# Kernel tuning notes

Measured on AMD Instinct MI355X. Metric: run time of the kernel, lower is better.

## Reference

```python
import jax, jax.numpy as jnp
import numpy as np

BLOCK_SIZE = 256
N_EMBD = 384
NUM_BLOCKS = 3
N_HEADS = 6
VOCAB_SIZE = 65
HEAD = N_EMBD // N_HEADS
EPS = 1e-5


def setup_inputs() -> dict:
    key = jax.random.key(0)
    ks = jax.random.split(key, 20)
    B, T = 64, 256
    s = 0.02
    L = NUM_BLOCKS
    inp = {
        "idx": jax.random.randint(ks[0], (B, T), 0, VOCAB_SIZE),
        "tok_emb": jax.random.normal(ks[1], (VOCAB_SIZE, N_EMBD), jnp.float32) * s,
        "pos_emb": jax.random.normal(ks[2], (BLOCK_SIZE, N_EMBD), jnp.float32) * s,
        "Wq": jax.random.normal(ks[3], (L, N_EMBD, N_EMBD), jnp.float32) * s,
        "Wk": jax.random.normal(ks[4], (L, N_EMBD, N_EMBD), jnp.float32) * s,
        "Wv": jax.random.normal(ks[5], (L, N_EMBD, N_EMBD), jnp.float32) * s,
        "Wo": jax.random.normal(ks[6], (L, N_EMBD, N_EMBD), jnp.float32) * s,
        "bo": jnp.zeros((L, N_EMBD), jnp.float32),
        "ln1_g": jnp.ones((L, N_EMBD), jnp.float32),
        "ln1_b": jnp.zeros((L, N_EMBD), jnp.float32),
        "ln2_g": jnp.ones((L, N_EMBD), jnp.float32),
        "ln2_b": jnp.zeros((L, N_EMBD), jnp.float32),
        "W1": jax.random.normal(ks[7], (L, N_EMBD, 4 * N_EMBD), jnp.float32) * s,
        "b1": jnp.zeros((L, 4 * N_EMBD), jnp.float32),
        "W2": jax.random.normal(ks[8], (L, 4 * N_EMBD, N_EMBD), jnp.float32) * s,
        "b2": jnp.zeros((L, N_EMBD), jnp.float32),
        "lnf_g": jnp.ones((N_EMBD,), jnp.float32),
        "lnf_b": jnp.zeros((N_EMBD,), jnp.float32),
        "Wlm": jax.random.normal(ks[9], (N_EMBD, VOCAB_SIZE), jnp.float32) * s,
        "blm": jnp.zeros((VOCAB_SIZE,), jnp.float32),
    }
    return inp


def _ln(x, g, b):
    m = jnp.mean(x, axis=-1, keepdims=True)
    v = jnp.mean((x - m) ** 2, axis=-1, keepdims=True)
    return (x - m) * jax.lax.rsqrt(v + EPS) * g + b


def reference(idx, tok_emb, pos_emb, Wq, Wk, Wv, Wo, bo, ln1_g, ln1_b,
              ln2_g, ln2_b, W1, b1, W2, b2, lnf_g, lnf_b, Wlm, blm):
    B, T = idx.shape
    x = tok_emb[idx] + pos_emb[:T]  # [B,T,C]
    scale = N_EMBD ** (-0.5)  # NOTE: original scales by full C=N_EMBD, not head_size
    causal = jnp.tril(jnp.ones((T, T), bool))
    neg_inf = jnp.finfo(x.dtype).min
    for l in range(NUM_BLOCKS):
        h = _ln(x, ln1_g[l], ln1_b[l])
        q = (h @ Wq[l]).reshape(B, T, N_HEADS, HEAD)
        k = (h @ Wk[l]).reshape(B, T, N_HEADS, HEAD)
        v = (h @ Wv[l]).reshape(B, T, N_HEADS, HEAD)
        wei = jnp.einsum("bthd,bshd->bhts", q, k) * scale
        wei = jnp.where(causal, wei, neg_inf)
        wei = jax.nn.softmax(wei, axis=-1)  # dropout is identity in eval
        att = jnp.einsum("bhts,bshd->bthd", wei, v).reshape(B, T, N_EMBD)
        x = x + att @ Wo[l] + bo[l]
        h2 = _ln(x, ln2_g[l], ln2_b[l])
        x = x + jax.nn.relu(h2 @ W1[l] + b1[l]) @ W2[l] + b2[l]
    x = _ln(x, lnf_g, lnf_b)
    logits = x @ Wlm + blm  # [B,T,V]
    return logits
```

## Files before the change

kernel.cpp:

```cpp
#include <hip/hip_runtime.h>

#define Bb 64
#define Tt 256
#define Cc 384
#define Ll 3
#define Hh 6
#define HD 64
#define Vv 65
#define FF 1536
#define NT (Bb*Tt)
#define CQ 1152
#define LDP 72

typedef unsigned short u16;
typedef unsigned int   u32;
typedef __attribute__((ext_vector_type(8))) short bf16x8;
typedef __attribute__((ext_vector_type(4))) float f32x4;

__device__ __forceinline__ float bf2f(u16 u) {
    u32 v = ((u32)u) << 16; float f; __builtin_memcpy(&f, &v, 4); return f;
}
__device__ __forceinline__ u16 f2bf(float f) {
    u32 u; __builtin_memcpy(&u, &f, 4);
    u = (u + 0x7fffu + ((u >> 16) & 1u)) >> 16;
    return (u16)u;
}
__device__ __forceinline__ void gload16(const void* g, void* l) {
    __builtin_amdgcn_global_load_lds(
        (const __attribute__((address_space(1))) u32*)g,
        (__attribute__((address_space(3))) u32*)l, 16, 0, 0);
}

__global__ __launch_bounds__(256) void k_embed_ln(const int* __restrict__ idx,
    const float* __restrict__ tok, const float* __restrict__ pos,
    const float* __restrict__ g, const float* __restrict__ b,
    float* __restrict__ x, u16* __restrict__ h)
{
    int bt   = (int)((blockIdx.x * 256 + threadIdx.x) >> 6);
    int lane = threadIdx.x & 63;
    int t = bt % Tt;
    const float* tr = tok + (long)idx[bt] * Cc;
    const float* pr = pos + (long)t * Cc;
    float v[6]; float s = 0.f;
    #pragma unroll
    for (int j = 0; j < 6; ++j) {
        int c = lane + 64 * j;
        v[j] = tr[c] + pr[c];
        s += v[j];
    }
    float* xr = x + (long)bt * Cc;
    #pragma unroll
    for (int j = 0; j < 6; ++j) xr[lane + 64 * j] = v[j];
    #pragma unroll
    for (int m = 32; m; m >>= 1) s += __shfl_xor(s, m, 64);
    float mean = s * (1.f / 384.f);
    float q = 0.f;
    #pragma unroll
    for (int j = 0; j < 6; ++j) { float d = v[j] - mean; q += d * d; }
    #pragma unroll
    for (int m = 32; m; m >>= 1) q += __shfl_xor(q, m, 64);
    float rstd = rsqrtf(q * (1.f / 384.f) + 1e-5f);
    u16* hr = h + (long)bt * Cc;
    #pragma unroll
    for (int j = 0; j < 6; ++j) {
        int c = lane + 64 * j;
        hr[c] = f2bf((v[j] - mean) * rstd * g[c] + b[c]);
    }
}

__global__ __launch_bounds__(256) void k_ln(const float* __restrict__ x,
    const float* __restrict__ g, const float* __restrict__ b, u16* __restrict__ h)
{
    int row  = (int)((blockIdx.x * 256 + threadIdx.x) >> 6);
    int lane = threadIdx.x & 63;
    const float* xr = x + (long)row * Cc;
    float v[6]; float s = 0.f;
    #pragma unroll
    for (int j = 0; j < 6; ++j) { v[j] = xr[lane + 64 * j]; s += v[j]; }
    #pragma unroll
    for (int m = 32; m; m >>= 1) s += __shfl_xor(s, m, 64);
    float mean = s * (1.f / 384.f);
    float q = 0.f;
    #pragma unroll
    for (int j = 0; j < 6; ++j) { float d = v[j] - mean; q += d * d; }
    #pragma unroll
    for (int m = 32; m; m >>= 1) q += __shfl_xor(q, m, 64);
    float rstd = rsqrtf(q * (1.f / 384.f) + 1e-5f);
    u16* hr = h + (long)row * Cc;
    #pragma unroll
    for (int j = 0; j < 6; ++j) {
        int c = lane + 64 * j;
        hr[c] = f2bf((v[j] - mean) * rstd * g[c] + b[c]);
    }
}

__global__ __launch_bounds__(256) void k_cvtT_all(
    const float* __restrict__ Wq, const float* __restrict__ Wk,
    const float* __restrict__ Wv, const float* __restrict__ Wo,
    const float* __restrict__ W1, const float* __restrict__ W2,
    u16* __restrict__ Wqkvt, u16* __restrict__ Wot,
    u16* __restrict__ W1t, u16* __restrict__ W2t)
{
    int t = blockIdx.x;
    const float* src; u16* dst; int K, N, tt;
    if (t < 1728) {
        int m = t / 144; tt = t % 144; K = Cc; N = Cc;
        if (m < 9) {
            int l = m / 3, q = m % 3;
            src = (q == 0 ? Wq : q == 1 ? Wk : Wv) + (size_t)l * Cc * Cc;
            dst = Wqkvt + (size_t)l * CQ * Cc + (size_t)q * Cc * Cc;
        } else {
            int l = m - 9;
            src = Wo + (size_t)l * Cc * Cc;
            dst = Wot + (size_t)l * Cc * Cc;
        }
    } else if (t < 3456) {
        int u = t - 1728; int l = u / 576; tt = u % 576; K = Cc; N = FF;
        src = W1 + (size_t)l * Cc * FF; dst = W1t + (size_t)l * FF * Cc;
    } else {
        int u = t - 3456; int l = u / 576; tt = u % 576; K = FF; N = Cc;
        src = W2 + (size_t)l * FF * Cc; dst = W2t + (size_t)l * Cc * FF;
    }
    int nk = K / 32;
    int kt = (tt % nk) * 32, nt = (tt / nk) * 32;
    __shared__ u16 tile[32][33];
    int tx = threadIdx.x & 31, ty = threadIdx.x >> 5;
    #pragma unroll
    for (int r = 0; r < 4; ++r)
        tile[ty + 8 * r][tx] = f2bf(src[(long)(kt + ty + 8 * r) * N + nt + tx]);
    __syncthreads();
    #pragma unroll
    for (int r = 0; r < 4; ++r)
        dst[(long)(nt + ty + 8 * r) * K + kt + tx] = tile[tx][ty + 8 * r];
}

__global__ void k_cvtT_lm(const float* __restrict__ W, u16* __restrict__ Wt)
{
    int i = blockIdx.x * 256 + threadIdx.x;
    if (i >= 128 * Cc) return;
    int k = i % Cc, n = i / Cc;
    Wt[i] = (n < Vv) ? f2bf(W[(long)k * Vv + n]) : (u16)0;
}

template<int EPI>
__global__ __launch_bounds__(256) void k_gemm128(
    const u16* __restrict__ A, const u16* __restrict__ Bt,
    const float* __restrict__ bias, void* __restrict__ Cout, int M, int N, int K)
{
    __shared__ __align__(16) u16 As[128 * 64];
    __shared__ __align__(16) u16 Bs[128 * 64];
    const int bm = blockIdx.x * 128;
    const int bn = blockIdx.y * 128;
    const int tid = threadIdx.x;
    const int lane = tid & 63, w = tid >> 6;
    const int wr = w >> 1, wc = w & 1;
    const int l15 = lane & 15, g = lane >> 4;
    const int lr = lane >> 3;
    const int lc = ((lane & 7) ^ lr) * 8;

    f32x4 acc[4][4] = {};
    const u16* Ag = A  + (long)(bm + w * 32 + lr) * K + lc;
    const u16* Bg = Bt + (long)(bn + w * 32 + lr) * K + lc;
    u16* Ad = As + (w * 4) * 512;
    u16* Bd = Bs + (w * 4) * 512;

    for (int k0 = 0; k0 < K; k0 += 64) {
        #pragma unroll
        for (int s = 0; s < 4; ++s) {
            gload16(Ag + (long)s * 8 * K + k0, Ad + s * 512);
            gload16(Bg + (long)s * 8 * K + k0, Bd + s * 512);
        }
        __syncthreads();
        #pragma unroll
        for (int hh = 0; hh < 2; ++hh) {
            const int cs = hh * 4 + g;
            bf16x8 af[4], bfr[4];
            #pragma unroll
            for (int mi = 0; mi < 4; ++mi) {
                int row = wr * 64 + mi * 16 + l15;
                af[mi] = *(const bf16x8*)((const char*)As + row * 128 + ((cs ^ (row & 7)) << 4));
            }
            #pragma unroll
            for (int ni = 0; ni < 4; ++ni) {
                int row = wc * 64 + ni * 16 + l15;
                bfr[ni] = *(const bf16x8*)((const char*)Bs + row * 128 + ((cs ^ (row & 7)) << 4));
            }
            #pragma unroll
            for (int mi = 0; mi < 4; ++mi)
            #pragma unroll
            for (int ni = 0; ni < 4; ++ni)
                acc[mi][ni] = __builtin_amdgcn_mfma_f32_16x16x32_bf16(af[mi], bfr[ni], acc[mi][ni], 0, 0, 0);
        }
        __syncthreads();
    }
    #pragma unroll
    for (int mi = 0; mi < 4; ++mi)
    #pragma unroll
    for (int ni = 0; ni < 4; ++ni)
    #pragma unroll
    for (int i = 0; i < 4; ++i) {
        int row = bm + wr * 64 + mi * 16 + g * 4 + i;
        int col = bn + wc * 64 + ni * 16 + l15;
        float v = acc[mi][ni][i];
        if constexpr (EPI == 1) v = fmaxf(v + bias[col], 0.f);
        ((u16*)Cout)[(long)row * N + col] = f2bf(v);
    }
}

template<int EPI>
__global__ __launch_bounds__(256) void k_gemm_n64(
    const u16* __restrict__ A, const u16* __restrict__ Bt,
    const float* __restrict__ bias, const float* __restrict__ R,
    void* __restrict__ Cout, int M, int N, int K, int Nout)
{
    __shared__ __align__(16) u16 As[128 * 64];
    __shared__ __align__(16) u16 Bs[64 * 64];
    const int bm = blockIdx.x * 128;
    const int bn = blockIdx.y * 64;
    const int tid = threadIdx.x;
    const int lane = tid & 63, w = tid >> 6;
    const int l15 = lane & 15, g = lane >> 4;
    const int lr = lane >> 3;
    const int lc = ((lane & 7) ^ lr) * 8;

    f32x4 acc[2][4] = {};
    const u16* Ag = A  + (long)(bm + w * 32 + lr) * K + lc;
    const u16* Bg = Bt + (long)(bn + w * 16 + lr) * K + lc;
    u16* Ad = As + (w * 4) * 512;
    u16* Bd = Bs + (w * 2) * 512;

    for (int k0 = 0; k0 < K; k0 += 64) {
        #pragma unroll
        for (int s = 0; s < 4; ++s)
            gload16(Ag + (long)s * 8 * K + k0, Ad + s * 512);
        #pragma unroll
        for (int t = 0; t < 2; ++t)
            gload16(Bg + (long)t * 8 * K + k0, Bd + t * 512);
        __syncthreads();
        #pragma unroll
        for (int hh = 0; hh < 2; ++hh) {
            const int cs = hh * 4 + g;
            bf16x8 af[2], bfr[4];
            #pragma unroll
            for (int mi = 0; mi < 2; ++mi) {
                int row = w * 32 + mi * 16 + l15;
                af[mi] = *(const bf16x8*)((const char*)As + row * 128 + ((cs ^ (row & 7)) << 4));
            }
            #pragma unroll
            for (int ni = 0; ni < 4; ++ni) {
                int row = ni * 16 + l15;
                bfr[ni] = *(const bf16x8*)((const char*)Bs + row * 128 + ((cs ^ (row & 7)) << 4));
            }
            #pragma unroll
            for (int mi = 0; mi < 2; ++mi)
            #pragma unroll
            for (int ni = 0; ni < 4; ++ni)
                acc[mi][ni] = __builtin_amdgcn_mfma_f32_16x16x32_bf16(af[mi], bfr[ni], acc[mi][ni], 0, 0, 0);
        }
        __syncthreads();
    }
    #pragma unroll
    for (int mi = 0; mi < 2; ++mi)
    #pragma unroll
    for (int ni = 0; ni < 4; ++ni)
    #pragma unroll
    for (int i = 0; i < 4; ++i) {
        int row = bm + w * 32 + mi * 16 + g * 4 + i;
        int col = bn + ni * 16 + l15;
        float v = acc[mi][ni][i];
        if constexpr (EPI == 2) {
            long o = (long)row * N + col;
            ((float*)Cout)[o] = v + bias[col] + R[o];
        } else {
            if (col < Nout)
                ((float*)Cout)[(long)row * Nout + col] = v + bias[col];
        }
    }
}

__global__ __launch_bounds__(256) void k_attn_mfma(const u16* __restrict__ qkv,
                                                   u16* __restrict__ att)
{
    __shared__ __align__(16) u16 ks[64][LDP];
    __shared__ __align__(16) u16 vt[64][LDP];
    __shared__ __align__(16) u16 pt[4][16][LDP];
    const int qt = blockIdx.x, hh = blockIdx.y, b = blockIdx.z;
    const int tid = threadIdx.x, lane = tid & 63, w = tid >> 6;
    const int l15 = lane & 15, g = lane >> 4;
    const int q0 = qt * 64;
    const long tokbase = (long)b * Tt;
    const float scale = 0.051031036307982884f;

    bf16x8 qa0, qa1;
    {
        const u16* qp = qkv + (tokbase + q0 + w * 16 + l15) * CQ + hh * HD + g * 8;
        qa0 = *(const bf16x8*)(qp);
        qa1 = *(const bf16x8*)(qp + 32);
    }
    f32x4 o[4] = {};
    float mrow[4] = {-1e30f, -1e30f, -1e30f, -1e30f};
    float lrow[4] = {0.f, 0.f, 0.f, 0.f};

    for (int kt = 0; kt <= qt; ++kt) {
        {
            int key = tid >> 2, c0 = (tid & 3) * 16;
            const u16* kg = qkv + (tokbase + kt * 64 + key) * CQ + Cc     + hh * HD + c0;
            const u16* vg = qkv + (tokbase + kt * 64 + key) * CQ + 2 * Cc + hh * HD + c0;
            *(bf16x8*)&ks[key][c0]     = *(const bf16x8*)kg;
            *(bf16x8*)&ks[key][c0 + 8] = *(const bf16x8*)(kg + 8);
            bf16x8 v0 = *(const bf16x8*)vg;
            bf16x8 v1 = *(const bf16x8*)(vg + 8);
            #pragma unroll
            for (int j = 0; j < 8; ++j) vt[c0 + j][key]     = (u16)v0[j];
            #pragma unroll
            for (int j = 0; j < 8; ++j) vt[c0 + 8 + j][key] = (u16)v1[j];
        }
        __syncthreads();
        f32x4 s[4] = {};
        #pragma unroll
        for (int c = 0; c < 4; ++c) {
            bf16x8 kb0 = *(const bf16x8*)&ks[c * 16 + l15][g * 8];
            bf16x8 kb1 = *(const bf16x8*)&ks[c * 16 + l15][32 + g * 8];
            s[c] = __builtin_amdgcn_mfma_f32_16x16x32_bf16(qa0, kb0, s[c], 0, 0, 0);
            s[c] = __builtin_amdgcn_mfma_f32_16x16x32_bf16(qa1, kb1, s[c], 0, 0, 0);
        }
        const bool diag = (kt == qt);
        #pragma unroll
        for (int c = 0; c < 4; ++c)
        #pragma unroll
        for (int i = 0; i < 4; ++i) {
            float v = s[c][i] * scale;
            if (diag && (c * 16 + l15 > w * 16 + 4 * g + i)) v = -1e30f;
            s[c][i] = v;
        }
        #pragma unroll
        for (int i = 0; i < 4; ++i) {
            float m0 = fmaxf(fmaxf(s[0][i], s[1][i]), fmaxf(s[2][i], s[3][i]));
            #pragma unroll
            for (int mm = 1; mm < 16; mm <<= 1) m0 = fmaxf(m0, __shfl_xor(m0, mm, 64));
            float mn = fmaxf(mrow[i], m0);
            float alpha = __expf(mrow[i] - mn);
            mrow[i] = mn;
            float sum = 0.f;
            #pragma unroll
            for (int c = 0; c < 4; ++c) {
                float p = __expf(s[c][i] - mn);
                s[c][i] = p;
                sum += p;
            }
            #pragma unroll
            for (int mm = 1; mm < 16; mm <<= 1) sum += __shfl_xor(sum, mm, 64);
            lrow[i] = lrow[i] * alpha + sum;
            #pragma unroll
            for (int d = 0; d < 4; ++d) o[d][i] *= alpha;
        }
        #pragma unroll
        for (int c = 0; c < 4; ++c)
        #pragma unroll
        for (int i = 0; i < 4; ++i)
            pt[w][g * 4 + i][c * 16 + l15] = f2bf(s[c][i]);
        bf16x8 pa0 = *(const bf16x8*)&pt[w][l15][g * 8];
        bf16x8 pa1 = *(const bf16x8*)&pt[w][l15][32 + g * 8];
        #pragma unroll
        for (int d = 0; d < 4; ++d) {
            bf16x8 vb0 = *(const bf16x8*)&vt[d * 16 + l15][g * 8];
            bf16x8 vb1 = *(const bf16x8*)&vt[d * 16 + l15][32 + g * 8];
            o[d] = __builtin_amdgcn_mfma_f32_16x16x32_bf16(pa0, vb0, o[d], 0, 0, 0);
            o[d] = __builtin_amdgcn_mfma_f32_16x16x32_bf16(pa1, vb1, o[d], 0, 0, 0);
        }
        __syncthreads();
    }
    #pragma unroll
    for (int i = 0; i < 4; ++i) {
        float inv = 1.f / lrow[i];
        int row = q0 + w * 16 + g * 4 + i;
        u16* ap = att + (tokbase + row) * Cc + hh * HD;
        #pragma unroll
        for (int d = 0; d < 4; ++d)
            ap[d * 16 + l15] = f2bf(o[d][i] * inv);
    }
}

extern "C" void kernel_launch(void* const* d_in, const int* in_sizes, int n_in,
                              void* d_out, int out_size, void* d_ws, size_t ws_size,
                              hipStream_t stream)
{
    (void)in_sizes; (void)n_in; (void)out_size; (void)ws_size;
    const int*   idx  = (const int*)d_in[0];
    const float* tok  = (const float*)d_in[1];
    const float* pos  = (const float*)d_in[2];
    const float* Wq   = (const float*)d_in[3];
    const float* Wk   = (const float*)d_in[4];
    const float* Wv   = (const float*)d_in[5];
    const float* Wo   = (const float*)d_in[6];
    const float* bo   = (const float*)d_in[7];
    const float* ln1g = (const float*)d_in[8];
    const float* ln1b = (const float*)d_in[9];
    const float* ln2g = (const float*)d_in[10];
    const float* ln2b = (const float*)d_in[11];
    const float* W1   = (const float*)d_in[12];
    const float* b1   = (const float*)d_in[13];
    const float* W2   = (const float*)d_in[14];
    const float* b2   = (const float*)d_in[15];
    const float* lnfg = (const float*)d_in[16];
    const float* lnfb = (const float*)d_in[17];
    const float* Wlm  = (const float*)d_in[18];
    const float* blm  = (const float*)d_in[19];

    char* w = (char*)d_ws;
    auto carve = [&](size_t bytes) { char* p = w; w += (bytes + 255) & ~(size_t)255; return p; };
    float* x   = (float*)carve((size_t)NT * Cc * 4);
    u16*  big  = (u16*)carve((size_t)NT * FF * 2);
    u16*  h    = (u16*)carve((size_t)NT * Cc * 2);
    u16*  ab   = (u16*)carve((size_t)NT * Cc * 2);
    u16*  Wqkvt= (u16*)carve((size_t)Ll * CQ * Cc * 2);
    u16*  Wot  = (u16*)carve((size_t)Ll * Cc * Cc * 2);
    u16*  W1t  = (u16*)carve((size_t)Ll * FF * Cc * 2);
    u16*  W2t  = (u16*)carve((size_t)Ll * Cc * FF * 2);
    u16*  Wlmt = (u16*)carve((size_t)128 * Cc * 2);
    u16*  qkvb = big;
    u16*  fb   = big;

    const int TPB = 256;
    k_cvtT_all<<<5184, TPB, 0, stream>>>(Wq, Wk, Wv, Wo, W1, W2, Wqkvt, Wot, W1t, W2t);
    k_cvtT_lm<<<(128 * Cc + 255) / 256, TPB, 0, stream>>>(Wlm, Wlmt);
    k_embed_ln<<<NT / 4, TPB, 0, stream>>>(idx, tok, pos, ln1g, ln1b, x, h);

    for (int l = 0; l < Ll; ++l) {
        if (l > 0)
            k_ln<<<NT / 4, TPB, 0, stream>>>(x, ln1g + l * Cc, ln1b + l * Cc, h);
        k_gemm128<0><<<dim3(NT / 128, CQ / 128), TPB, 0, stream>>>(
            h, Wqkvt + (size_t)l * CQ * Cc, nullptr, qkvb, NT, CQ, Cc);
        k_attn_mfma<<<dim3(4, Hh, Bb), TPB, 0, stream>>>(qkvb, ab);
        k_gemm_n64<2><<<dim3(NT / 128, Cc / 64), TPB, 0, stream>>>(
            ab, Wot + (size_t)l * Cc * Cc, bo + l * Cc, x, x, NT, Cc, Cc, Cc);
        k_ln<<<NT / 4, TPB, 0, stream>>>(x, ln2g + l * Cc, ln2b + l * Cc, h);
        k_gemm128<1><<<dim3(NT / 128, FF / 128), TPB, 0, stream>>>(
            h, W1t + (size_t)l * FF * Cc, b1 + l * FF, fb, NT, FF, Cc);
        k_gemm_n64<2><<<dim3(NT / 128, Cc / 64), TPB, 0, stream>>>(
            fb, W2t + (size_t)l * Cc * FF, b2 + l * Cc, x, x, NT, Cc, FF, Cc);
    }
    k_ln<<<NT / 4, TPB, 0, stream>>>(x, lnfg, lnfb, h);
    k_gemm_n64<3><<<dim3(NT / 128, 2), TPB, 0, stream>>>(
        h, Wlmt, blm, nullptr, (float*)d_out, NT, 128, Cc, Vv);
}
```

Before: 453.2 us.

## Double-buffer LDS tiles in 128x128 GEMM with async prefetch two steps ahead

Splits the shared-memory A/B tiles of the 128x128 GEMM into two buffers and issues the global-to-LDS loads for tile t+2 while tile t is being computed. Manual vmcnt waits and raw s_barrier replace __syncthreads, so the global load latency can overlap with the MFMA work. In exchange LDS use doubles to 64 KB per block, which may lower occupancy, and the hand-written waitcnt counts must match the number of outstanding loads per stage.

```diff
diff --git a/kernel.cpp b/kernel.cpp
--- a/kernel.cpp
+++ b/kernel.cpp
@@ -147,8 +147,8 @@
     const u16* __restrict__ A, const u16* __restrict__ Bt,
     const float* __restrict__ bias, void* __restrict__ Cout, int M, int N, int K)
 {
-    __shared__ __align__(16) u16 As[128 * 64];
-    __shared__ __align__(16) u16 Bs[128 * 64];
+    __shared__ __align__(16) u16 As[2][128 * 64];
+    __shared__ __align__(16) u16 Bs[2][128 * 64];
     const int bm = blockIdx.x * 128;
     const int bn = blockIdx.y * 128;
     const int tid = threadIdx.x;
@@ -161,16 +161,26 @@
     f32x4 acc[4][4] = {};
     const u16* Ag = A  + (long)(bm + w * 32 + lr) * K + lc;
     const u16* Bg = Bt + (long)(bn + w * 32 + lr) * K + lc;
-    u16* Ad = As + (w * 4) * 512;
-    u16* Bd = Bs + (w * 4) * 512;
-
-    for (int k0 = 0; k0 < K; k0 += 64) {
+
+    auto stage = [&](int buf, int k0) {
+        u16* Ad = As[buf] + (w * 4) * 512;
+        u16* Bd = Bs[buf] + (w * 4) * 512;
         #pragma unroll
         for (int s = 0; s < 4; ++s) {
             gload16(Ag + (long)s * 8 * K + k0, Ad + s * 512);
             gload16(Bg + (long)s * 8 * K + k0, Bd + s * 512);
         }
-        __syncthreads();
+    };
+    const int nt = K / 64;
+    stage(0, 0);
+    if (nt > 1) stage(1, 64);
+    for (int t = 0; t < nt; ++t) {
+        if (t < nt - 1) asm volatile("s_waitcnt vmcnt(8)" ::: "memory");
+        else            asm volatile("s_waitcnt vmcnt(0)" ::: "memory");
+        __builtin_amdgcn_s_barrier();
+        asm volatile("" ::: "memory");
+        const char* Abuf = (const char*)As[t & 1];
+        const char* Bbuf = (const char*)Bs[t & 1];
         #pragma unroll
         for (int hh = 0; hh < 2; ++hh) {
             const int cs = hh * 4 + g;
@@ -178,12 +188,12 @@
             #pragma unroll
             for (int mi = 0; mi < 4; ++mi) {
                 int row = wr * 64 + mi * 16 + l15;
-                af[mi] = *(const bf16x8*)((const char*)As + row * 128 + ((cs ^ (row & 7)) << 4));
+                af[mi] = *(const bf16x8*)(Abuf + row * 128 + ((cs ^ (row & 7)) << 4));
             }
             #pragma unroll
             for (int ni = 0; ni < 4; ++ni) {
                 int row = wc * 64 + ni * 16 + l15;
-                bfr[ni] = *(const bf16x8*)((const char*)Bs + row * 128 + ((cs ^ (row & 7)) << 4));
+                bfr[ni] = *(const bf16x8*)(Bbuf + row * 128 + ((cs ^ (row & 7)) << 4));
             }
             #pragma unroll
             for (int mi = 0; mi < 4; ++mi)
@@ -191,7 +201,9 @@
             for (int ni = 0; ni < 4; ++ni)
                 acc[mi][ni] = __builtin_amdgcn_mfma_f32_16x16x32_bf16(af[mi], bfr[ni], acc[mi][ni], 0, 0, 0);
         }
-        __syncthreads();
+        asm volatile("" ::: "memory");
+        __builtin_amdgcn_s_barrier();
+        if (t + 2 < nt) stage(t & 1, (t + 2) * 64);
     }
     #pragma unroll
     for (int mi = 0; mi < 4; ++mi)
```

After: 446.6 us. Within noise of the previous version (-1.5%).
